# Performance work log

Measured on AMD Instinct MI355X. Metric: run time of the kernel, lower is better.

The kernel has to match this reference:

```python
import jax, jax.numpy as jnp
import numpy as np

EPS = 1e-5

def _lstm_scan(x, mask, Wih, Whh, bih, bhh):
    # x: [B,T,D], mask: [B,T] float (applied to h and c AFTER each step, like the torch code)
    B, T, _ = x.shape
    H = Whh.shape[1]
    x_t = jnp.swapaxes(x, 0, 1)            # [T,B,D]
    m_t = jnp.swapaxes(mask, 0, 1)[:, :, None]  # [T,B,1]
    bias = bih + bhh
    def step(carry, inp):
        h, c = carry
        xt, mt = inp
        gates = xt @ Wih.T + h @ Whh.T + bias   # [B,4H], torch gate order i,f,g,o
        i, f, g, o = jnp.split(gates, 4, axis=-1)
        c = jax.nn.sigmoid(f) * c + jax.nn.sigmoid(i) * jnp.tanh(g)
        h = jax.nn.sigmoid(o) * jnp.tanh(c)
        h = h * mt
        c = c * mt
        return (h, c), h
    h0 = jnp.zeros((B, H), x.dtype)
    _, ys = jax.lax.scan(step, (h0, h0), (x_t, m_t))
    return jnp.swapaxes(ys, 0, 1)          # [B,T,H]

def _layernorm(x, g, b):
    mu = x.mean(-1, keepdims=True)
    var = ((x - mu) ** 2).mean(-1, keepdims=True)
    return (x - mu) * jax.lax.rsqrt(var + EPS) * g + b

def setup_inputs() -> dict:
    key = jax.random.key(0)
    ks = jax.random.split(key, 18)
    B, T, D, H, C = 64, 512, 256, 512, 1000
    def u(k, shape, fan):
        s = 1.0 / np.sqrt(fan)
        return jax.random.uniform(k, shape, jnp.float32, -s, s)
    x = jax.random.normal(ks[0], (B, T, D), jnp.float32)
    reset_mask = jax.random.randint(ks[1], (B, T), 0, 2).astype(jnp.float32)
    return {
        "x": x, "reset_mask": reset_mask,
        # layer 0 LSTM (torch init: U(-1/sqrt(H), 1/sqrt(H)))
        "Wih0": u(ks[2], (4 * H, D), H), "Whh0": u(ks[3], (4 * H, H), H),
        "bih0": u(ks[4], (4 * H,), H), "bhh0": u(ks[5], (4 * H,), H),
        "g0": jnp.ones((H,), jnp.float32), "beta0": jnp.zeros((H,), jnp.float32),
        # layer 1 LSTM
        "Wih1": u(ks[6], (4 * H, H), H), "Whh1": u(ks[7], (4 * H, H), H),
        "bih1": u(ks[8], (4 * H,), H), "bhh1": u(ks[9], (4 * H,), H),
        "g1": jnp.ones((H,), jnp.float32), "beta1": jnp.zeros((H,), jnp.float32),
        # final classifier
        "fcW": u(ks[10], (C, H), H), "fcb": u(ks[11], (C,), H),
    }

def reference(x, reset_mask, Wih0, Whh0, bih0, bhh0, g0, beta0,
              Wih1, Whh1, bih1, bhh1, g1, beta1, fcW, fcb):
    h = _lstm_scan(x, reset_mask, Wih0, Whh0, bih0, bhh0)
    h = _layernorm(jax.nn.relu(h), g0, beta0)
    h = _lstm_scan(h, reset_mask, Wih1, Whh1, bih1, bhh1)
    h = _layernorm(jax.nn.relu(h), g1, beta1)
    return h[:, -1, :] @ fcW.T + fcb        # [B, num_classes]
```

## Files before the change

### kernel.cpp

```cpp
#include <hip/hip_runtime.h>
#include <stdint.h>

#define BB 64
#define TT 512
#define DD 256
#define HH 512
#define NG 2048
#define BT (BB*TT)
#define NCLS 1000
#define MAXS 16

typedef _Float16 f16;
typedef _Float16 f16x2 __attribute__((ext_vector_type(2)));
typedef _Float16 f16x4 __attribute__((ext_vector_type(4)));
typedef _Float16 f16x8 __attribute__((ext_vector_type(8)));
typedef float f32x4 __attribute__((ext_vector_type(4)));

__device__ const int d_OFF[MAXS] = {0,32768,49152,60096,68288,74880,80384,85120,
                                    89216,92864,96192,99200,101952,104512,106880,109120};

__device__ __forceinline__ float sigf(float x) { return 1.0f / (1.0f + __expf(-x)); }
__device__ __forceinline__ float tanh_(float x) {
  float e = __expf(-2.0f * fabsf(x));
  float r = (1.0f - e) / (1.0f + e);
  return copysignf(r, x);
}
__device__ __forceinline__ f32x4 mfma16(f16x8 a, f16x8 b, f32x4 c) {
  return __builtin_amdgcn_mfma_f32_16x16x32_f16(a, b, c, 0, 0, 0);
}
__device__ __forceinline__ void gload16(const void* g, void* l) {
  __builtin_amdgcn_global_load_lds((const __attribute__((address_space(1))) void*)g,
                                   (__attribute__((address_space(3))) void*)l, 16, 0, 0);
}

#define C0 (NG*DD/4)
#define C1 (C0 + NG*HH/4)
#define C2 (C1 + NG*HH/4)
#define C3 (C2 + NG*HH/4)
#define CX (C3 + BT*DD/4)
__global__ __launch_bounds__(256) void prep_weights(
    const float* __restrict__ Wih0, const float* __restrict__ Whh0,
    const float* __restrict__ Wih1, const float* __restrict__ Whh1,
    const float* __restrict__ x,
    const float* __restrict__ bih0, const float* __restrict__ bhh0,
    const float* __restrict__ bih1, const float* __restrict__ bhh1,
    f16* __restrict__ W16ih0, f16* __restrict__ W16hh0,
    f16* __restrict__ W16ih1, f16* __restrict__ W16hh1,
    f16* __restrict__ AX,
    float* __restrict__ bias0, float* __restrict__ bias1) {
  int gi = blockIdx.x * 256 + threadIdx.x;
  for (int i = gi; i < CX; i += gridDim.x * 256) {
    const float* s; f16* d; int o;
    if (i < C0)      { s = Wih0; d = W16ih0; o = i; }
    else if (i < C1) { s = Whh0; d = W16hh0; o = i - C0; }
    else if (i < C2) { s = Wih1; d = W16ih1; o = i - C1; }
    else if (i < C3) { s = Whh1; d = W16hh1; o = i - C2; }
    else             { s = x;    d = AX;     o = i - C3; }
    float4 v = ((const float4*)s)[o];
    f16x4 h = { (f16)v.x, (f16)v.y, (f16)v.z, (f16)v.w };
    ((f16x4*)d)[o] = h;
  }
  if (gi < NG/2) {
    int j = gi * 2;
    bias0[j]   = bih0[j]   + bhh0[j];
    bias0[j+1] = bih0[j+1] + bhh0[j+1];
    bias1[j]   = bih1[j]   + bhh1[j];
    bias1[j+1] = bih1[j+1] + bhh1[j+1];
  }
}

__global__ __launch_bounds__(512) void build_lists(const float* __restrict__ mask,
    int* __restrict__ counts, int* __restrict__ lists,
    int* __restrict__ tailcnt, int* __restrict__ taillist) {
  int b = blockIdx.x, t = threadIdx.x;
  __shared__ float sm[512];
  __shared__ int lcnt[MAXS], lbase[MAXS];
  sm[t] = mask[b*TT + t];
  if (t < MAXS) lcnt[t] = 0;
  __syncthreads();
  int run = 0;
  for (int j = 1; j <= MAXS; ++j) {
    if (t - j < 0) break;
    if (sm[t - j] != 0.0f) run++; else break;
  }
  bool tail = (run >= MAXS);
  int slot = -1;
  if (!tail) slot = atomicAdd(&lcnt[run], 1);
  __syncthreads();
  if (t < MAXS) lbase[t] = atomicAdd(&counts[t*32], lcnt[t]);
  __syncthreads();
  if (!tail) lists[d_OFF[run] + lbase[run] + slot] = b*TT + t;
  unsigned long long bal = __ballot(tail);
  int lane = t & 63, w = t >> 6;
  int wpre = __popcll(bal & ((1ull << lane) - 1ull));
  __shared__ int wsum[8];
  if (lane == 0) wsum[w] = __popcll(bal);
  __syncthreads();
  int base = 0;
  for (int i = 0; i < w; ++i) base += wsum[i];
  if (tail) taillist[b*TT + base + wpre] = t;
  if (t == 0) {
    int tot = 0;
    for (int i = 0; i < 8; ++i) tot += wsum[i];
    tailcnt[b] = tot;
  }
}

__global__ __launch_bounds__(256) void proj_gemm(const f16* __restrict__ A,
    const f16* __restrict__ W, const float* __restrict__ bias,
    f16* __restrict__ C, int K) {
  __shared__ __align__(16) f16 smem[128*128];
  f16* As = smem;
  f16* Bs = smem + 128*64;
  const int nwg = gridDim.x;
  const int cpx = nwg >> 3;
  const int b0i = blockIdx.x;
  const int swz = (b0i & 7) * cpx + (b0i >> 3);
  const int m0 = (swz >> 4) * 128;
  const int n0 = (swz & 15) * 128;
  const int tid = threadIdx.x;
  const int lane = tid & 63;
  const int w = tid >> 6;
  const int srg = lane >> 3;
  const int scol = lane & 7;
  f32x4 acc[4][4] = {};
  for (int k0 = 0; k0 < K; k0 += 64) {
#pragma unroll
    for (int i = 0; i < 4; ++i) {
      int r0 = (i*4 + w) * 8;
      int row = r0 + srg;
      int cg = scol ^ (row & 7);
      gload16(A + (size_t)(m0 + row)*K + k0 + cg*8, As + r0*64);
      gload16(W + (size_t)(n0 + row)*K + k0 + cg*8, Bs + r0*64);
    }
    __syncthreads();
    {
      const int wm = (w >> 1) * 64;
      const int wn = (w & 1) * 64;
      const int cl = lane & 15;
      const int kq = lane >> 4;
#pragma unroll
      for (int ks = 0; ks < 2; ++ks) {
        int kc = ks*4 + kq;
        f16x8 af[4], bf[4];
#pragma unroll
        for (int mi = 0; mi < 4; ++mi) {
          int row = wm + mi*16 + cl;
          af[mi] = *(const f16x8*)(As + row*64 + ((kc ^ (row & 7)) * 8));
        }
#pragma unroll
        for (int ni = 0; ni < 4; ++ni) {
          int row = wn + ni*16 + cl;
          bf[ni] = *(const f16x8*)(Bs + row*64 + ((kc ^ (row & 7)) * 8));
        }
#pragma unroll
        for (int mi = 0; mi < 4; ++mi)
#pragma unroll
          for (int ni = 0; ni < 4; ++ni)
            acc[mi][ni] = mfma16(af[mi], bf[ni], acc[mi][ni]);
      }
    }
    __syncthreads();
  }
  {
    const int wm = (w >> 1) * 64;
    const int wn = (w & 1) * 64;
    const int cl = lane & 15;
    const int rq = lane >> 4;
#pragma unroll
    for (int ni = 0; ni < 4; ++ni) {
      int col = wn + ni*16 + cl;
      float bb = bias[n0 + col];
#pragma unroll
      for (int mi = 0; mi < 4; ++mi)
#pragma unroll
        for (int r = 0; r < 4; ++r)
          smem[(wm + mi*16 + rq*4 + r)*128 + col] = (f16)(acc[mi][ni][r] + bb);
    }
  }
  __syncthreads();
#pragma unroll
  for (int p = 0; p < 8; ++p) {
    int row = p*16 + (tid >> 4);
    int ch = tid & 15;
    f16x8 v = *(const f16x8*)(smem + row*128 + ch*8);
    *(f16x8*)(C + (size_t)(m0 + row)*NG + n0 + ch*8) = v;
  }
}

__global__ __launch_bounds__(512) void lstm_step0(const f16* __restrict__ G,
    f16* __restrict__ HS, f16* __restrict__ CS, const float* __restrict__ mask,
    const int* __restrict__ counts, const int* __restrict__ lists) {
  int cnt = counts[0];
  int i = blockIdx.x * 4 + (threadIdx.x >> 7);
  if (i >= cnt) return;
  int row = lists[i];
  int j4 = (threadIdx.x & 127) * 4;
  size_t gb = (size_t)row * NG;
  f16x4 vi = *(const f16x4*)(G + gb + j4);
  f16x4 vg = *(const f16x4*)(G + gb + 1024 + j4);
  f16x4 vo = *(const f16x4*)(G + gb + 1536 + j4);
  float m = mask[row];
  f16x4 hv, cv;
#pragma unroll
  for (int e = 0; e < 4; ++e) {
    float c = sigf((float)vi[e]) * tanh_((float)vg[e]);
    float h = sigf((float)vo[e]) * tanh_(c);
    hv[e] = (f16)(h*m); cv[e] = (f16)(c*m);
  }
  *(f16x4*)(HS + (size_t)row*HH + j4) = hv;
  *(f16x4*)(CS + (size_t)row*HH + j4) = cv;
}

__global__ __launch_bounds__(512) void lstm_step(const f16* __restrict__ Wh,
    const f16* __restrict__ G, f16* __restrict__ HS, f16* __restrict__ CS,
    const float* __restrict__ mask, const int* __restrict__ counts,
    const int* __restrict__ lists, int s) {
  const int cnt = counts[s*32];
  if (cnt == 0) return;
  const int units = ((cnt + 127) >> 7) * 8;
  const int* lst = lists + d_OFF[s];
  const int tid = threadIdx.x;
  const int lane = tid & 63;
  const int w = tid >> 6;
  __shared__ __align__(16) f16 As[128*64];
  __shared__ __align__(16) f16 Bs[256*64];
  __shared__ int ridx[128];
  __shared__ float rmk[128];
  const int rg = w >> 2;
  const int jg = w & 3;
  const int cl = lane & 15;
  const int kq = lane >> 4;

  for (int u = blockIdx.x; u < units; u += gridDim.x) {
    const int mbase = (u >> 3) * 128;
    const int j0 = (u & 7) * 64;
    if (tid < 128) {
      int i = mbase + tid;
      int r = (i < cnt) ? lst[i] : -1;
      ridx[tid] = r;
      rmk[tid] = (r >= 0) ? mask[r] : 0.0f;
    }
    __syncthreads();

    const f16* asrc[2];
#pragma unroll
    for (int p = 0; p < 2; ++p) {
      int cid = tid + p*512;
      int r = cid >> 3, c = cid & 7;
      int cs = c ^ (r & 7);
      int rr = ridx[r];
      int sr = (rr >= 1 ? rr : 1) - 1;
      asrc[p] = HS + (size_t)sr*HH + cs*8;
    }
    const f16* bsrc[4];
#pragma unroll
    for (int p = 0; p < 4; ++p) {
      int cid = tid + p*512;
      int grow = cid >> 3, c = cid & 7;
      int cs = c ^ (grow & 7);
      int wrow = (grow >> 6)*512 + j0 + (grow & 63);
      bsrc[p] = Wh + (size_t)wrow*HH + cs*8;
    }

    f32x4 acc[4][4] = {};
    for (int k0 = 0; k0 < HH; k0 += 64) {
#pragma unroll
      for (int p = 0; p < 2; ++p)
        gload16(asrc[p] + k0, As + (tid + p*512)*8);
#pragma unroll
      for (int p = 0; p < 4; ++p)
        gload16(bsrc[p] + k0, Bs + (tid + p*512)*8);
      __syncthreads();
#pragma unroll
      for (int ks = 0; ks < 2; ++ks) {
        int kc = ks*4 + kq;
        f16x8 af[4], bf[4];
#pragma unroll
        for (int mi = 0; mi < 4; ++mi) {
          int row = rg*64 + mi*16 + cl;
          af[mi] = *(const f16x8*)(As + row*64 + ((kc ^ (row & 7))*8));
        }
#pragma unroll
        for (int g = 0; g < 4; ++g) {
          int brow = g*64 + jg*16 + cl;
          bf[g] = *(const f16x8*)(Bs + brow*64 + ((kc ^ (brow & 7))*8));
        }
#pragma unroll
        for (int mi = 0; mi < 4; ++mi)
#pragma unroll
          for (int g = 0; g < 4; ++g)
            acc[mi][g] = mfma16(af[mi], bf[g], acc[mi][g]);
      }
      __syncthreads();
    }

    const int j = j0 + jg*16 + cl;
#pragma unroll
    for (int mi = 0; mi < 4; ++mi)
#pragma unroll
      for (int r = 0; r < 4; ++r) {
        int slot = rg*64 + mi*16 + kq*4 + r;
        int row = ridx[slot];
        if (row >= 0) {
          size_t gb = (size_t)row * NG;
          float gi = acc[mi][0][r] + (float)G[gb + j];
          float gf = acc[mi][1][r] + (float)G[gb + 512 + j];
          float gg = acc[mi][2][r] + (float)G[gb + 1024 + j];
          float go = acc[mi][3][r] + (float)G[gb + 1536 + j];
          float cp = (float)CS[(size_t)(row - 1)*HH + j];
          float c = sigf(gf)*cp + sigf(gi)*tanh_(gg);
          float h = sigf(go)*tanh_(c);
          float m = rmk[slot];
          HS[(size_t)row*HH + j] = (f16)(h*m);
          CS[(size_t)row*HH + j] = (f16)(c*m);
        }
      }
    __syncthreads();
  }
}

__global__ __launch_bounds__(512) void lstm_step_thin(const f16* __restrict__ Wh,
    const f16* __restrict__ G, f16* __restrict__ HS, f16* __restrict__ CS,
    const float* __restrict__ mask, const int* __restrict__ counts,
    const int* __restrict__ lists, int s) {
  const int cnt = counts[s*32];
  if (cnt == 0) return;
  const int units = ((cnt + 127) >> 7) * 32;
  const int* lst = lists + d_OFF[s];
  const int tid = threadIdx.x;
  const int lane = tid & 63;
  const int w = tid >> 6;
  __shared__ __align__(16) f16 As[128*64];
  __shared__ __align__(16) f16 Bs[64*64];
  __shared__ int ridx[128];
  __shared__ float rmk[128];
  const int cl = lane & 15;
  const int kq = lane >> 4;
  const int rbase = w * 16;

  for (int u = blockIdx.x; u < units; u += gridDim.x) {
    const int mbase = (u >> 5) * 128;
    const int j0 = (u & 31) * 16;
    if (tid < 128) {
      int i = mbase + tid;
      int r = (i < cnt) ? lst[i] : -1;
      ridx[tid] = r;
      rmk[tid] = (r >= 0) ? mask[r] : 0.0f;
    }
    __syncthreads();

    const f16* asrc[2];
#pragma unroll
    for (int p = 0; p < 2; ++p) {
      int cid = tid + p*512;
      int r = cid >> 3, c = cid & 7;
      int cs = c ^ (r & 7);
      int rr = ridx[r];
      int sr = (rr >= 1 ? rr : 1) - 1;
      asrc[p] = HS + (size_t)sr*HH + cs*8;
    }
    const f16* bsrc;
    {
      int grow = tid >> 3, c = tid & 7;
      int cs = c ^ (grow & 7);
      int wrow = (grow >> 4)*512 + j0 + (grow & 15);
      bsrc = Wh + (size_t)wrow*HH + cs*8;
    }

    f32x4 acc[4] = {};
    for (int k0 = 0; k0 < HH; k0 += 64) {
#pragma unroll
      for (int p = 0; p < 2; ++p)
        gload16(asrc[p] + k0, As + (tid + p*512)*8);
      gload16(bsrc + k0, Bs + tid*8);
      __syncthreads();
#pragma unroll
      for (int ks = 0; ks < 2; ++ks) {
        int kc = ks*4 + kq;
        int arow = rbase + cl;
        f16x8 af = *(const f16x8*)(As + arow*64 + ((kc ^ (arow & 7))*8));
        f16x8 bf[4];
#pragma unroll
        for (int g = 0; g < 4; ++g) {
          int brow = g*16 + cl;
          bf[g] = *(const f16x8*)(Bs + brow*64 + ((kc ^ (brow & 7))*8));
        }
#pragma unroll
        for (int g = 0; g < 4; ++g)
          acc[g] = mfma16(af, bf[g], acc[g]);
      }
      __syncthreads();
    }

    const int j = j0 + cl;
#pragma unroll
    for (int r = 0; r < 4; ++r) {
      int slot = rbase + kq*4 + r;
      int row = ridx[slot];
      if (row >= 0) {
        size_t gb = (size_t)row * NG;
        float gi = acc[0][r] + (float)G[gb + j];
        float gf = acc[1][r] + (float)G[gb + 512 + j];
        float gg = acc[2][r] + (float)G[gb + 1024 + j];
        float go = acc[3][r] + (float)G[gb + 1536 + j];
        float cp = (float)CS[(size_t)(row - 1)*HH + j];
        float c = sigf(gf)*cp + sigf(gi)*tanh_(gg);
        float h = sigf(go)*tanh_(c);
        float m = rmk[slot];
        HS[(size_t)row*HH + j] = (f16)(h*m);
        CS[(size_t)row*HH + j] = (f16)(c*m);
      }
    }
    __syncthreads();
  }
}

__global__ __launch_bounds__(512) void lstm_tail(const f16* __restrict__ Wh,
    const f16* __restrict__ G, f16* __restrict__ HS, f16* __restrict__ CS,
    const float* __restrict__ mask, const int* __restrict__ tailcnt,
    const int* __restrict__ taillist) {
  int b = blockIdx.x;
  int n = tailcnt[b];
  if (n == 0) return;
  int tid = threadIdx.x, lane = tid & 63, w = tid >> 6;
  const int rl = lane >> 3;
  const int kb = (lane & 7) * 8;
  __shared__ __align__(16) f16 hsh[HH];
  __shared__ float gsh[NG];
  for (int i = 0; i < n; ++i) {
    int t = taillist[b*TT + i];
    size_t row = (size_t)b*TT + t;
    if (tid < 256)
      ((uint32_t*)hsh)[tid] = ((const uint32_t*)(HS + (row - 1)*HH))[tid];
    __syncthreads();
    f16x8 hreg[8];
#pragma unroll
    for (int kk = 0; kk < 8; ++kk)
      hreg[kk] = *(const f16x8*)(hsh + kb + kk*64);
#pragma unroll 2
    for (int batch = 0; batch < 32; ++batch) {
      int o = (w*32 + batch)*8 + rl;
      const f16* wrow = Wh + (size_t)o*HH + kb;
      float p = 0.0f;
#pragma unroll
      for (int kk = 0; kk < 8; ++kk) {
        f16x8 wv = *(const f16x8*)(wrow + kk*64);
        f16x2 w0 = {wv[0], wv[1]}, w1 = {wv[2], wv[3]}, w2 = {wv[4], wv[5]}, w3 = {wv[6], wv[7]};
        f16x2 h0 = {hreg[kk][0], hreg[kk][1]}, h1 = {hreg[kk][2], hreg[kk][3]},
              h2 = {hreg[kk][4], hreg[kk][5]}, h3 = {hreg[kk][6], hreg[kk][7]};
        p = __builtin_amdgcn_fdot2(w0, h0, p, false);
        p = __builtin_amdgcn_fdot2(w1, h1, p, false);
        p = __builtin_amdgcn_fdot2(w2, h2, p, false);
        p = __builtin_amdgcn_fdot2(w3, h3, p, false);
      }
      p += __shfl_xor(p, 1);
      p += __shfl_xor(p, 2);
      p += __shfl_xor(p, 4);
      if ((lane & 7) == 0) gsh[o] = p + (float)G[row*NG + o];
    }
    __syncthreads();
    {
      float cp = (float)CS[(row - 1)*HH + tid];
      float c = sigf(gsh[512 + tid])*cp + sigf(gsh[tid])*tanh_(gsh[1024 + tid]);
      float h = sigf(gsh[1536 + tid])*tanh_(c);
      float m = mask[row];
      HS[row*HH + tid] = (f16)(h*m);
      CS[row*HH + tid] = (f16)(c*m);
    }
    __syncthreads();
  }
}

__global__ __launch_bounds__(512) void ln_relu(const f16* __restrict__ in,
    const float* __restrict__ g, const float* __restrict__ be,
    f16* __restrict__ out) {
  int lane = threadIdx.x & 63, w = threadIdx.x >> 6;
  int row = blockIdx.x * 8 + w;
  f16x8 hv = *(const f16x8*)(in + (size_t)row*HH + lane*8);
  float xv[8]; float s1 = 0.f, s2 = 0.f;
#pragma unroll
  for (int e = 0; e < 8; ++e) { float x = fmaxf((float)hv[e], 0.f); xv[e] = x; s1 += x; s2 += x*x; }
#pragma unroll
  for (int o = 1; o < 64; o <<= 1) { s1 += __shfl_xor(s1, o); s2 += __shfl_xor(s2, o); }
  float mu = s1 * (1.0f/512.0f);
  float var = s2 * (1.0f/512.0f) - mu*mu;
  float rs = rsqrtf(var + 1e-5f);
  f16x8 ov;
#pragma unroll
  for (int e = 0; e < 8; ++e) ov[e] = (f16)((xv[e] - mu)*rs*g[lane*8+e] + be[lane*8+e]);
  *(f16x8*)(out + (size_t)row*HH + lane*8) = ov;
}

__global__ __launch_bounds__(512) void ln_last(const f16* __restrict__ HS,
    const float* __restrict__ g, const float* __restrict__ be, float* __restrict__ out) {
  int b = blockIdx.x;
  int j = threadIdx.x;
  float x = fmaxf((float)HS[((size_t)b*TT + (TT-1))*HH + j], 0.0f);
  float s1 = x, s2 = x*x;
  for (int o = 32; o > 0; o >>= 1) { s1 += __shfl_down(s1, o); s2 += __shfl_down(s2, o); }
  __shared__ float a1[8], a2[8];
  int w = j >> 6;
  if ((j & 63) == 0) { a1[w] = s1; a2[w] = s2; }
  __syncthreads();
  if (j == 0) {
    float t1 = 0.f, t2 = 0.f;
    for (int i = 0; i < 8; ++i) { t1 += a1[i]; t2 += a2[i]; }
    a1[0] = t1; a2[0] = t2;
  }
  __syncthreads();
  float mu = a1[0] * (1.0f/512.0f);
  float var = a2[0] * (1.0f/512.0f) - mu*mu;
  float y = (x - mu) * rsqrtf(var + 1e-5f) * g[j] + be[j];
  out[b*HH + j] = y;
}

__global__ __launch_bounds__(256) void fc_kernel(const float* __restrict__ hf,
    const float* __restrict__ W, const float* __restrict__ bias, float* __restrict__ out) {
  int b = blockIdx.y;
  int c = blockIdx.x * 256 + threadIdx.x;
  __shared__ float hsh[512];
  hsh[threadIdx.x] = hf[b*HH + threadIdx.x];
  hsh[threadIdx.x + 256] = hf[b*HH + 256 + threadIdx.x];
  __syncthreads();
  if (c < NCLS) {
    const float4* wr = (const float4*)(W + (size_t)c*HH);
    float acc = bias[c];
#pragma unroll 4
    for (int k4 = 0; k4 < 128; ++k4) {
      float4 wv = wr[k4];
      acc += wv.x*hsh[k4*4] + wv.y*hsh[k4*4+1] + wv.z*hsh[k4*4+2] + wv.w*hsh[k4*4+3];
    }
    out[b*NCLS + c] = acc;
  }
}

extern "C" void kernel_launch(void* const* d_in, const int* in_sizes, int n_in,
                              void* d_out, int out_size, void* d_ws, size_t ws_size,
                              hipStream_t stream) {
  (void)in_sizes; (void)n_in; (void)out_size;
  const float* x    = (const float*)d_in[0];
  const float* mask = (const float*)d_in[1];
  const float* Wih0 = (const float*)d_in[2];
  const float* Whh0 = (const float*)d_in[3];
  const float* bih0 = (const float*)d_in[4];
  const float* bhh0 = (const float*)d_in[5];
  const float* g0   = (const float*)d_in[6];
  const float* be0  = (const float*)d_in[7];
  const float* Wih1 = (const float*)d_in[8];
  const float* Whh1 = (const float*)d_in[9];
  const float* bih1 = (const float*)d_in[10];
  const float* bhh1 = (const float*)d_in[11];
  const float* g1   = (const float*)d_in[12];
  const float* be1  = (const float*)d_in[13];
  const float* fcW  = (const float*)d_in[14];
  const float* fcb  = (const float*)d_in[15];
  float* out = (float*)d_out;

  char* ws = (char*)d_ws;
  size_t off = 0;
  auto alloc = [&](size_t bytes) { size_t o = off; off += (bytes + 255) & ~(size_t)255; return o; };
  f16* G      = (f16*)(ws + alloc((size_t)BT*NG*2));
  f16* HS     = (f16*)(ws + alloc((size_t)BT*HH*2));
  f16* CS     = (f16*)(ws + alloc((size_t)BT*HH*2));
  f16* H0LN   = (f16*)(ws + alloc((size_t)BT*HH*2));
  f16* W16ih0 = (f16*)(ws + alloc((size_t)NG*DD*2));
  f16* W16hh0 = (f16*)(ws + alloc((size_t)NG*HH*2));
  f16* W16ih1 = (f16*)(ws + alloc((size_t)NG*HH*2));
  f16* W16hh1 = (f16*)(ws + alloc((size_t)NG*HH*2));
  float* bias0 = (float*)(ws + alloc(NG*4));
  float* bias1 = (float*)(ws + alloc(NG*4));
  int* counts  = (int*)(ws + alloc(4096));
  int* tailcnt = counts + 512;
  int* lists   = (int*)(ws + alloc(111168*4));
  int* taillist= (int*)(ws + alloc((size_t)BT*4));
  float* hf    = (float*)(ws + alloc((size_t)BB*HH*4));
  if (ws_size < off) return;

  f16* AX = H0LN;

  hipMemsetAsync(counts, 0, 4096, stream);
  prep_weights<<<dim3(512), dim3(256), 0, stream>>>(Wih0, Whh0, Wih1, Whh1, x,
      bih0, bhh0, bih1, bhh1, W16ih0, W16hh0, W16ih1, W16hh1, AX, bias0, bias1);
  build_lists<<<dim3(BB), dim3(512), 0, stream>>>(mask, counts, lists, tailcnt, taillist);

  for (int layer = 0; layer < 2; ++layer) {
    const f16* Wih16 = layer ? W16ih1 : W16ih0;
    const f16* Whh16 = layer ? W16hh1 : W16hh0;
    const float* bias = layer ? bias1 : bias0;
    const f16* Ain = layer ? H0LN : AX;
    int K = layer ? HH : DD;
    proj_gemm<<<dim3((BT/128)*(NG/128)), dim3(256), 0, stream>>>(Ain, Wih16, bias, G, K);
    lstm_step0<<<dim3(BT/4), dim3(512), 0, stream>>>(G, HS, CS, mask, counts, lists);
    for (int s = 1; s < 5; ++s)
      lstm_step<<<dim3(512), dim3(512), 0, stream>>>(Whh16, G, HS, CS, mask, counts, lists, s);
    for (int s = 5; s < MAXS; ++s)
      lstm_step_thin<<<dim3(256), dim3(512), 0, stream>>>(Whh16, G, HS, CS, mask, counts, lists, s);
    lstm_tail<<<dim3(BB), dim3(512), 0, stream>>>(Whh16, G, HS, CS, mask, tailcnt, taillist);
    if (layer == 0)
      ln_relu<<<dim3(BT/8), dim3(512), 0, stream>>>(HS, g0, be0, H0LN);
  }

  ln_last<<<dim3(BB), dim3(512), 0, stream>>>(HS, g1, be1, hf);
  fc_kernel<<<dim3(4, BB), dim3(256), 0, stream>>>(hf, fcW, fcb, out);
}
```

Measured before the change: 845.3 us.

## Fuse step-0 LSTM activation into input projection GEMM and vectorize step epilogue

The input projection GEMM is retiled so each block computes all four gates for a 64-wide hidden slice. Rows with no recurrent dependency (run==0) get their LSTM cell activation applied directly in the epilogue, which writes H/C and skips the G write. Other rows still store G as before. This removes the separate lstm_step0 kernel and the G round-trip for those rows, about half of all rows. The recurrent lstm_step epilogue is also restaged through shared memory so G, C and H are read and written as 8-wide vectors instead of scalars, at the cost of extra barriers and shared-memory traffic.

Result: faster. 804.0 us (-4.9%).

```diff
diff --git a/kernel.cpp b/kernel.cpp
--- a/kernel.cpp
+++ b/kernel.cpp
@@ -71,7 +71,8 @@
 
 __global__ __launch_bounds__(512) void build_lists(const float* __restrict__ mask,
     int* __restrict__ counts, int* __restrict__ lists,
-    int* __restrict__ tailcnt, int* __restrict__ taillist) {
+    int* __restrict__ tailcnt, int* __restrict__ taillist,
+    float* __restrict__ selm) {
   int b = blockIdx.x, t = threadIdx.x;
   __shared__ float sm[512];
   __shared__ int lcnt[MAXS], lbase[MAXS];
@@ -83,13 +84,14 @@
     if (t - j < 0) break;
     if (sm[t - j] != 0.0f) run++; else break;
   }
+  selm[b*TT + t] = (run == 0) ? sm[t] : -1.0f;
   bool tail = (run >= MAXS);
   int slot = -1;
-  if (!tail) slot = atomicAdd(&lcnt[run], 1);
+  if (!tail && run > 0) slot = atomicAdd(&lcnt[run], 1);
   __syncthreads();
   if (t < MAXS) lbase[t] = atomicAdd(&counts[t*32], lcnt[t]);
   __syncthreads();
-  if (!tail) lists[d_OFF[run] + lbase[run] + slot] = b*TT + t;
+  if (!tail && run > 0) lists[d_OFF[run] + lbase[run] + slot] = b*TT + t;
   unsigned long long bal = __ballot(tail);
   int lane = t & 63, w = t >> 6;
   int wpre = __popcll(bal & ((1ull << lane) - 1ull));
@@ -106,110 +108,134 @@
   }
 }
 
-__global__ __launch_bounds__(256) void proj_gemm(const f16* __restrict__ A,
+__global__ __launch_bounds__(512) void proj_act(const f16* __restrict__ A,
     const f16* __restrict__ W, const float* __restrict__ bias,
-    f16* __restrict__ C, int K) {
-  __shared__ __align__(16) f16 smem[128*128];
+    f16* __restrict__ G, f16* __restrict__ HS, f16* __restrict__ CS,
+    const float* __restrict__ selm, int K) {
+  __shared__ __align__(16) f16 smem[128*64 + 256*64];
   f16* As = smem;
   f16* Bs = smem + 128*64;
+  __shared__ float sel[128];
   const int nwg = gridDim.x;
   const int cpx = nwg >> 3;
-  const int b0i = blockIdx.x;
-  const int swz = (b0i & 7) * cpx + (b0i >> 3);
-  const int m0 = (swz >> 4) * 128;
-  const int n0 = (swz & 15) * 128;
+  const int swz = (blockIdx.x & 7) * cpx + (blockIdx.x >> 3);
+  const int m0 = (swz >> 3) * 128;
+  const int j0 = (swz & 7) * 64;
   const int tid = threadIdx.x;
   const int lane = tid & 63;
   const int w = tid >> 6;
-  const int srg = lane >> 3;
-  const int scol = lane & 7;
+  if (tid < 128) sel[tid] = selm[m0 + tid];
+
+  const f16* asrc[2];
+#pragma unroll
+  for (int p = 0; p < 2; ++p) {
+    int cid = tid + p*512;
+    int r = cid >> 3, c = cid & 7;
+    int cs = c ^ (r & 7);
+    asrc[p] = A + (size_t)(m0 + r)*K + cs*8;
+  }
+  const f16* bsrc[4];
+#pragma unroll
+  for (int p = 0; p < 4; ++p) {
+    int cid = tid + p*512;
+    int grow = cid >> 3, c = cid & 7;
+    int cs = c ^ (grow & 7);
+    int wrow = (grow >> 6)*512 + j0 + (grow & 63);
+    bsrc[p] = W + (size_t)wrow*K + cs*8;
+  }
+
+  const int rg = w >> 2;
+  const int jg = w & 3;
+  const int cl = lane & 15;
+  const int kq = lane >> 4;
   f32x4 acc[4][4] = {};
+
   for (int k0 = 0; k0 < K; k0 += 64) {
 #pragma unroll
-    for (int i = 0; i < 4; ++i) {
-      int r0 = (i*4 + w) * 8;
-      int row = r0 + srg;
-      int cg = scol ^ (row & 7);
-      gload16(A + (size_t)(m0 + row)*K + k0 + cg*8, As + r0*64);
-      gload16(W + (size_t)(n0 + row)*K + k0 + cg*8, Bs + r0*64);
+    for (int p = 0; p < 2; ++p)
+      gload16(asrc[p] + k0, As + (tid + p*512)*8);
+#pragma unroll
+    for (int p = 0; p < 4; ++p)
+      gload16(bsrc[p] + k0, Bs + (tid + p*512)*8);
+    __syncthreads();
+#pragma unroll
+    for (int ks = 0; ks < 2; ++ks) {
+      int kc = ks*4 + kq;
+      f16x8 af[4], bf[4];
+#pragma unroll
+      for (int mi = 0; mi < 4; ++mi) {
+        int row = rg*64 + mi*16 + cl;
+        af[mi] = *(const f16x8*)(As + row*64 + ((kc ^ (row & 7))*8));
+      }
+#pragma unroll
+      for (int g = 0; g < 4; ++g) {
+        int brow = g*64 + jg*16 + cl;
+        bf[g] = *(const f16x8*)(Bs + brow*64 + ((kc ^ (brow & 7))*8));
+      }
+#pragma unroll
+      for (int mi = 0; mi < 4; ++mi)
+#pragma unroll
+        for (int g = 0; g < 4; ++g)
+          acc[mi][g] = mfma16(af[mi], bf[g], acc[mi][g]);
+    }
+    __syncthreads();
+  }
+
+  const int j = j0 + jg*16 + cl;
+#pragma unroll
+  for (int g = 0; g < 4; ++g) {
+    float bb = bias[g*512 + j];
+#pragma unroll
+    for (int mi = 0; mi < 4; ++mi)
+#pragma unroll
+      for (int r = 0; r < 4; ++r)
+        acc[mi][g][r] += bb;
+  }
+
+  f16* stg = smem;
+#pragma unroll
+  for (int half = 0; half < 2; ++half) {
+    if (rg == half) {
+#pragma unroll
+      for (int mi = 0; mi < 4; ++mi)
+#pragma unroll
+        for (int g = 0; g < 4; ++g)
+#pragma unroll
+          for (int r = 0; r < 4; ++r) {
+            int row_l = mi*16 + kq*4 + r;
+            stg[row_l*264 + g*64 + jg*16 + cl] = (f16)acc[mi][g][r];
+          }
     }
     __syncthreads();
     {
-      const int wm = (w >> 1) * 64;
-      const int wn = (w & 1) * 64;
-      const int cl = lane & 15;
-      const int kq = lane >> 4;
-#pragma unroll
-      for (int ks = 0; ks < 2; ++ks) {
-        int kc = ks*4 + kq;
-        f16x8 af[4], bf[4];
-#pragma unroll
-        for (int mi = 0; mi < 4; ++mi) {
-          int row = wm + mi*16 + cl;
-          af[mi] = *(const f16x8*)(As + row*64 + ((kc ^ (row & 7)) * 8));
+      int row_l = tid >> 3, sl = tid & 7;
+      int slot = half*64 + row_l;
+      int row = m0 + slot;
+      int jj = j0 + sl*8;
+      f16x8 vi = *(const f16x8*)(stg + row_l*264 +        sl*8);
+      f16x8 vf = *(const f16x8*)(stg + row_l*264 +  64 + sl*8);
+      f16x8 vg = *(const f16x8*)(stg + row_l*264 + 128 + sl*8);
+      f16x8 vo = *(const f16x8*)(stg + row_l*264 + 192 + sl*8);
+      float sm = sel[slot];
+      if (sm >= 0.0f) {
+        f16x8 hv, cv;
+#pragma unroll
+        for (int e = 0; e < 8; ++e) {
+          float c = sigf((float)vi[e]) * tanh_((float)vg[e]);
+          float h = sigf((float)vo[e]) * tanh_(c);
+          hv[e] = (f16)(h*sm); cv[e] = (f16)(c*sm);
         }
-#pragma unroll
-        for (int ni = 0; ni < 4; ++ni) {
-          int row = wn + ni*16 + cl;
-          bf[ni] = *(const f16x8*)(Bs + row*64 + ((kc ^ (row & 7)) * 8));
-        }
-#pragma unroll
-        for (int mi = 0; mi < 4; ++mi)
-#pragma unroll
-          for (int ni = 0; ni < 4; ++ni)
-            acc[mi][ni] = mfma16(af[mi], bf[ni], acc[mi][ni]);
-      }
-    }
-    __syncthreads();
-  }
-  {
-    const int wm = (w >> 1) * 64;
-    const int wn = (w & 1) * 64;
-    const int cl = lane & 15;
-    const int rq = lane >> 4;
-#pragma unroll
-    for (int ni = 0; ni < 4; ++ni) {
-      int col = wn + ni*16 + cl;
-      float bb = bias[n0 + col];
-#pragma unroll
-      for (int mi = 0; mi < 4; ++mi)
-#pragma unroll
-        for (int r = 0; r < 4; ++r)
-          smem[(wm + mi*16 + rq*4 + r)*128 + col] = (f16)(acc[mi][ni][r] + bb);
-    }
-  }
-  __syncthreads();
-#pragma unroll
-  for (int p = 0; p < 8; ++p) {
-    int row = p*16 + (tid >> 4);
-    int ch = tid & 15;
-    f16x8 v = *(const f16x8*)(smem + row*128 + ch*8);
-    *(f16x8*)(C + (size_t)(m0 + row)*NG + n0 + ch*8) = v;
-  }
-}
-
-__global__ __launch_bounds__(512) void lstm_step0(const f16* __restrict__ G,
-    f16* __restrict__ HS, f16* __restrict__ CS, const float* __restrict__ mask,
-    const int* __restrict__ counts, const int* __restrict__ lists) {
-  int cnt = counts[0];
-  int i = blockIdx.x * 4 + (threadIdx.x >> 7);
-  if (i >= cnt) return;
-  int row = lists[i];
-  int j4 = (threadIdx.x & 127) * 4;
-  size_t gb = (size_t)row * NG;
-  f16x4 vi = *(const f16x4*)(G + gb + j4);
-  f16x4 vg = *(const f16x4*)(G + gb + 1024 + j4);
-  f16x4 vo = *(const f16x4*)(G + gb + 1536 + j4);
-  float m = mask[row];
-  f16x4 hv, cv;
-#pragma unroll
-  for (int e = 0; e < 4; ++e) {
-    float c = sigf((float)vi[e]) * tanh_((float)vg[e]);
-    float h = sigf((float)vo[e]) * tanh_(c);
-    hv[e] = (f16)(h*m); cv[e] = (f16)(c*m);
-  }
-  *(f16x4*)(HS + (size_t)row*HH + j4) = hv;
-  *(f16x4*)(CS + (size_t)row*HH + j4) = cv;
+        *(f16x8*)(HS + (size_t)row*HH + jj) = hv;
+        *(f16x8*)(CS + (size_t)row*HH + jj) = cv;
+      } else {
+        *(f16x8*)(G + (size_t)row*NG +        jj) = vi;
+        *(f16x8*)(G + (size_t)row*NG +  512 + jj) = vf;
+        *(f16x8*)(G + (size_t)row*NG + 1024 + jj) = vg;
+        *(f16x8*)(G + (size_t)row*NG + 1536 + jj) = vo;
+      }
+    }
+    __syncthreads();
+  }
 }
 
 __global__ __launch_bounds__(512) void lstm_step(const f16* __restrict__ Wh,
@@ -223,8 +249,9 @@
   const int tid = threadIdx.x;
   const int lane = tid & 63;
   const int w = tid >> 6;
-  __shared__ __align__(16) f16 As[128*64];
-  __shared__ __align__(16) f16 Bs[256*64];
+  __shared__ __align__(16) f16 smem[128*64 + 256*64];
+  f16* As = smem;
+  f16* Bs = smem + 128*64;
   __shared__ int ridx[128];
   __shared__ float rmk[128];
   const int rg = w >> 2;
@@ -295,28 +322,54 @@
       __syncthreads();
     }
 
-    const int j = j0 + jg*16 + cl;
-#pragma unroll
-    for (int mi = 0; mi < 4; ++mi)
-#pragma unroll
-      for (int r = 0; r < 4; ++r) {
-        int slot = rg*64 + mi*16 + kq*4 + r;
+    f16* stg = smem;
+#pragma unroll
+    for (int half = 0; half < 2; ++half) {
+      if (rg == half) {
+#pragma unroll
+        for (int mi = 0; mi < 4; ++mi)
+#pragma unroll
+          for (int g = 0; g < 4; ++g)
+#pragma unroll
+            for (int r = 0; r < 4; ++r) {
+              int row_l = mi*16 + kq*4 + r;
+              stg[row_l*264 + g*64 + jg*16 + cl] = (f16)acc[mi][g][r];
+            }
+      }
+      __syncthreads();
+      {
+        int row_l = tid >> 3, sl = tid & 7;
+        int slot = half*64 + row_l;
         int row = ridx[slot];
         if (row >= 0) {
-          size_t gb = (size_t)row * NG;
-          float gi = acc[mi][0][r] + (float)G[gb + j];
-          float gf = acc[mi][1][r] + (float)G[gb + 512 + j];
-          float gg = acc[mi][2][r] + (float)G[gb + 1024 + j];
-          float go = acc[mi][3][r] + (float)G[gb + 1536 + j];
-          float cp = (float)CS[(size_t)(row - 1)*HH + j];
-          float c = sigf(gf)*cp + sigf(gi)*tanh_(gg);
-          float h = sigf(go)*tanh_(c);
+          int jj = j0 + sl*8;
+          f16x8 ai = *(const f16x8*)(stg + row_l*264 +        sl*8);
+          f16x8 af2 = *(const f16x8*)(stg + row_l*264 +  64 + sl*8);
+          f16x8 ag = *(const f16x8*)(stg + row_l*264 + 128 + sl*8);
+          f16x8 ao = *(const f16x8*)(stg + row_l*264 + 192 + sl*8);
+          f16x8 Gi = *(const f16x8*)(G + (size_t)row*NG +        jj);
+          f16x8 Gf = *(const f16x8*)(G + (size_t)row*NG +  512 + jj);
+          f16x8 Gg = *(const f16x8*)(G + (size_t)row*NG + 1024 + jj);
+          f16x8 Go = *(const f16x8*)(G + (size_t)row*NG + 1536 + jj);
+          f16x8 cp = *(const f16x8*)(CS + (size_t)(row - 1)*HH + jj);
           float m = rmk[slot];
-          HS[(size_t)row*HH + j] = (f16)(h*m);
-          CS[(size_t)row*HH + j] = (f16)(c*m);
+          f16x8 hv, cv;
+#pragma unroll
+          for (int e = 0; e < 8; ++e) {
+            float gi = (float)ai[e] + (float)Gi[e];
+            float gf = (float)af2[e] + (float)Gf[e];
+            float gg = (float)ag[e] + (float)Gg[e];
+            float go = (float)ao[e] + (float)Go[e];
+            float c = sigf(gf)*(float)cp[e] + sigf(gi)*tanh_(gg);
+            float h = sigf(go)*tanh_(c);
+            hv[e] = (f16)(h*m); cv[e] = (f16)(c*m);
+          }
+          *(f16x8*)(HS + (size_t)row*HH + jj) = hv;
+          *(f16x8*)(CS + (size_t)row*HH + jj) = cv;
         }
       }
-    __syncthreads();
+      __syncthreads();
+    }
   }
 }
 
@@ -574,6 +627,7 @@
   int* tailcnt = counts + 512;
   int* lists   = (int*)(ws + alloc(111168*4));
   int* taillist= (int*)(ws + alloc((size_t)BT*4));
+  float* selm  = (float*)(ws + alloc((size_t)BT*4));
   float* hf    = (float*)(ws + alloc((size_t)BB*HH*4));
   if (ws_size < off) return;
 
@@ -582,7 +636,7 @@
   hipMemsetAsync(counts, 0, 4096, stream);
   prep_weights<<<dim3(512), dim3(256), 0, stream>>>(Wih0, Whh0, Wih1, Whh1, x,
       bih0, bhh0, bih1, bhh1, W16ih0, W16hh0, W16ih1, W16hh1, AX, bias0, bias1);
-  build_lists<<<dim3(BB), dim3(512), 0, stream>>>(mask, counts, lists, tailcnt, taillist);
+  build_lists<<<dim3(BB), dim3(512), 0, stream>>>(mask, counts, lists, tailcnt, taillist, selm);
 
   for (int layer = 0; layer < 2; ++layer) {
     const f16* Wih16 = layer ? W16ih1 : W16ih0;
@@ -590,8 +644,7 @@
     const float* bias = layer ? bias1 : bias0;
     const f16* Ain = layer ? H0LN : AX;
     int K = layer ? HH : DD;
-    proj_gemm<<<dim3((BT/128)*(NG/128)), dim3(256), 0, stream>>>(Ain, Wih16, bias, G, K);
-    lstm_step0<<<dim3(BT/4), dim3(512), 0, stream>>>(G, HS, CS, mask, counts, lists);
+    proj_act<<<dim3((BT/128)*8), dim3(512), 0, stream>>>(Ain, Wih16, bias, G, HS, CS, selm, K);
     for (int s = 1; s < 5; ++s)
       lstm_step<<<dim3(512), dim3(512), 0, stream>>>(Whh16, G, HS, CS, mask, counts, lists, s);
     for (int s = 5; s < MAXS; ++s)
```
